# Performance work log

Measured on AMD Instinct MI355X. Metric: run time of the kernel, lower is better.

The kernel has to match this reference:

```python
import jax, jax.numpy as jnp
import numpy as np

N = 50000          # nodes
E = 400000         # random edges (self-loops added in reference, per PyG default)
IN, HID, HEADS, OUT = 20, 64, 4, 256
NEG_SLOPE = 0.2    # GATv2Conv default negative_slope
EPS = 1e-16        # PyG softmax denom epsilon


def setup_inputs() -> dict:
    key = jax.random.key(0)
    ks = jax.random.split(key, 14)
    g = lambda k, shape, scale=0.1: (jax.random.normal(k, shape, jnp.float32) * scale)
    return {
        "x": jax.random.normal(ks[0], (N, IN), jnp.float32),
        "edge_index": jax.random.randint(ks[1], (2, E), 0, N, jnp.int32),
        # layer 1: GATv2Conv(IN -> HID, heads=HEADS, concat=True)
        "W_l1": g(ks[2], (IN, HEADS * HID)),
        "b_l1": jnp.zeros((HEADS * HID,), jnp.float32),
        "W_r1": g(ks[3], (IN, HEADS * HID)),
        "b_r1": jnp.zeros((HEADS * HID,), jnp.float32),
        "att1": g(ks[4], (HEADS, HID)),
        "bias1": jnp.zeros((HEADS * HID,), jnp.float32),
        # layer 2: GATv2Conv(HEADS*HID -> OUT, heads=1, concat=False)
        "W_l2": g(ks[5], (HEADS * HID, OUT)),
        "b_l2": jnp.zeros((OUT,), jnp.float32),
        "W_r2": g(ks[6], (HEADS * HID, OUT)),
        "b_r2": jnp.zeros((OUT,), jnp.float32),
        "att2": g(ks[7], (1, OUT)),
        "bias2": jnp.zeros((OUT,), jnp.float32),
    }


def _gatv2_layer(x, src, dst, W_l, b_l, W_r, b_r, att, bias, heads, ch, concat):
    n = x.shape[0]
    x_l = (x @ W_l + b_l).reshape(n, heads, ch)  # source transform
    x_r = (x @ W_r + b_r).reshape(n, heads, ch)  # target transform
    # GATv2: e_ij = att . LeakyReLU(x_l[j] + x_r[i])   (j->i edge)
    pre = jax.nn.leaky_relu(x_l[src] + x_r[dst], NEG_SLOPE)       # [E, H, C]
    logits = jnp.einsum('ehc,hc->eh', pre, att)                    # [E, H]
    # segment softmax over destination node (self-loops guarantee nonempty)
    m = jax.ops.segment_max(logits, dst, num_segments=n)
    w = jnp.exp(logits - m[dst])
    denom = jax.ops.segment_sum(w, dst, num_segments=n)
    alpha = w / (denom[dst] + EPS)                                 # [E, H]
    out = jax.ops.segment_sum(x_l[src] * alpha[:, :, None], dst, num_segments=n)
    out = out.reshape(n, heads * ch) if concat else out.mean(axis=1)
    return out + bias


def reference(x, edge_index, W_l1, b_l1, W_r1, b_r1, att1, bias1,
              W_l2, b_l2, W_r2, b_r2, att2, bias2):
    n = x.shape[0]
    loop = jnp.arange(n, dtype=edge_index.dtype)  # PyG add_self_loops=True
    src = jnp.concatenate([edge_index[0], loop])
    dst = jnp.concatenate([edge_index[1], loop])
    h = _gatv2_layer(x, src, dst, W_l1, b_l1, W_r1, b_r1, att1, bias1, HEADS, HID, True)
    h = jax.nn.elu(h)
    out = _gatv2_layer(h, src, dst, W_l2, b_l2, W_r2, b_r2, att2, bias2, 1, OUT, False)
    return out
```

## Files before the change

kernel.cpp:

```cpp
#include <hip/hip_runtime.h>
#include <math.h>

#define CH 256
#define SCAN_BLOCK 1024
#define LOG2E 1.44269504088896f

typedef _Float16 h2 __attribute__((ext_vector_type(2)));
typedef _Float16 h4 __attribute__((ext_vector_type(4)));
typedef _Float16 f16x8 __attribute__((ext_vector_type(8)));
typedef float f32x4 __attribute__((ext_vector_type(4)));

__device__ __forceinline__ float elu(float v)   { return v > 0.f ? v : __expf(v) - 1.f; }

__device__ __forceinline__ unsigned short f2h(float f) {
    union { _Float16 h; unsigned short u; } c;
    c.h = (_Float16)f;
    return c.u;
}

__device__ __forceinline__ float edge_logit(h4 r, h2 xrlo, h2 xrhi, h2 alo, h2 ahi) {
    const h2 k = {(_Float16)0.2f, (_Float16)0.2f};
    h2 rlo = {r.x, r.y}, rhi = {r.z, r.w};
    h2 slo = rlo + xrlo;
    h2 shi = rhi + xrhi;
    slo = __builtin_elementwise_max(slo, slo * k);
    shi = __builtin_elementwise_max(shi, shi * k);
    float p = __builtin_amdgcn_fdot2(slo, alo, 0.f, false);
    return __builtin_amdgcn_fdot2(shi, ahi, p, false);
}

template<int C>
__device__ __forceinline__ float dppadd(float v) {
    int t = __builtin_amdgcn_update_dpp(0, __float_as_int(v), C, 0xf, 0xf, true);
    return v + __int_as_float(t);
}
__device__ __forceinline__ float red16(float p) {
    p = dppadd<0xB1>(p);
    p = dppadd<0x4E>(p);
    p = dppadd<0x141>(p);
    p = dppadd<0x140>(p);
    return p;
}
__device__ __forceinline__ float red64(float p) {
    p = red16(p);
    p += __shfl_xor(p, 16);
    p += __shfl_xor(p, 32);
    return p;
}

typedef const __attribute__((address_space(1))) unsigned int* gas_p;
typedef __attribute__((address_space(3))) unsigned int* las_p;
__device__ __forceinline__ void gload16(const unsigned short* g, unsigned short* l) {
    __builtin_amdgcn_global_load_lds((gas_p)g, (las_p)l, 16, 0, 0);
}

__global__ __launch_bounds__(256) void gemm1_kernel(const float* __restrict__ x,
                             const float* __restrict__ Wl, const float* __restrict__ bl,
                             const float* __restrict__ Wr, const float* __restrict__ br,
                             unsigned short* __restrict__ xl, unsigned short* __restrict__ xr, int n) {
    __shared__ float xs[64][20];
    int n0 = blockIdx.x * 64;
    int tid = threadIdx.x;
    for (int i = tid; i < 64 * 20; i += 256) {
        int m = i / 20, k = i % 20;
        int row = n0 + m;
        xs[m][k] = (row < n) ? x[(size_t)row * 20 + k] : 0.f;
    }
    int c = tid;
    float wl[20], wr[20];
#pragma unroll
    for (int k = 0; k < 20; ++k) { wl[k] = Wl[k * 256 + c]; wr[k] = Wr[k * 256 + c]; }
    float blv = bl[c], brv = br[c];
    __syncthreads();
#pragma unroll 1
    for (int g = 0; g < 8; ++g) {
        int base = g * 8;
        float al[8], ar[8];
#pragma unroll
        for (int m = 0; m < 8; ++m) { al[m] = blv; ar[m] = brv; }
#pragma unroll
        for (int k = 0; k < 20; ++k) {
            float wlv = wl[k], wrv = wr[k];
#pragma unroll
            for (int m = 0; m < 8; ++m) {
                float xv = xs[base + m][k];
                al[m] += xv * wlv;
                ar[m] += xv * wrv;
            }
        }
#pragma unroll
        for (int m = 0; m < 8; ++m) {
            int row = n0 + base + m;
            if (row < n) {
                xl[(size_t)row * 256 + c] = f2h(al[m]);
                xr[(size_t)row * 256 + c] = f2h(ar[m]);
            }
        }
    }
}

__global__ void count_deg(const int* __restrict__ ei, int* __restrict__ deg, int e) {
    int t = blockIdx.x * blockDim.x + threadIdx.x;
    if (t < e) atomicAdd(&deg[ei[e + t]], 1);
}

__global__ void scan_block_k(const int* __restrict__ deg, int* __restrict__ rowptr,
                             int* __restrict__ bsums, int n) {
    __shared__ int wsum[16];
    __shared__ int woff[17];
    int tid = threadIdx.x;
    int gi = blockIdx.x * SCAN_BLOCK + tid;
    int lane = tid & 63, wid = tid >> 6;
    int v = (gi < n) ? deg[gi] : 0;
    int incl = v;
#pragma unroll
    for (int d = 1; d < 64; d <<= 1) {
        int t = __shfl_up(incl, d, 64);
        if (lane >= d) incl += t;
    }
    if (lane == 63) wsum[wid] = incl;
    __syncthreads();
    if (tid < 16) {
        int s = wsum[tid];
#pragma unroll
        for (int d = 1; d < 16; d <<= 1) {
            int t = __shfl_up(s, d, 64);
            if (tid >= d) s += t;
        }
        woff[tid + 1] = s;
        if (tid == 0) woff[0] = 0;
    }
    __syncthreads();
    incl += woff[wid];
    if (gi < n) rowptr[gi + 1] = incl;
    if (tid == 0) bsums[blockIdx.x] = woff[16];
}

__global__ void scan_tops_k(int* bsums, int nb) {
    int tid = threadIdx.x;
    int v = (tid < nb) ? bsums[tid] : 0;
    int incl = v;
#pragma unroll
    for (int d = 1; d < 64; d <<= 1) {
        int t = __shfl_up(incl, d, 64);
        if (tid >= d) incl += t;
    }
    if (tid < nb) bsums[tid] = incl - v;
}

__global__ void scan_fix_k(int* __restrict__ rowptr, int* __restrict__ cursor,
                           const int* __restrict__ deg, const int* __restrict__ bsums, int n) {
    int gi = blockIdx.x * SCAN_BLOCK + threadIdx.x;
    if (gi >= n) return;
    int off = bsums[blockIdx.x];
    int incl = rowptr[gi + 1] + off;
    rowptr[gi + 1] = incl;
    cursor[gi] = incl - deg[gi];
    if (gi == 0) rowptr[0] = 0;
}

__global__ void scatter_k(const int* __restrict__ ei, int* __restrict__ cursor,
                          int* __restrict__ csr, int e) {
    int t = blockIdx.x * blockDim.x + threadIdx.x;
    if (t >= e) return;
    int s = ei[t], d = ei[e + t];
    int idx = atomicAdd(&cursor[d], 1);
    csr[idx] = s;
}

__global__ void fused_gat1(const unsigned short* __restrict__ xl, const unsigned short* __restrict__ xr,
                           const int* __restrict__ rowptr, const int* __restrict__ csr,
                           const float* __restrict__ att, const float* __restrict__ bias,
                           unsigned short* __restrict__ hout, int n) {
    int wid = threadIdx.x >> 6;
    int lane = threadIdx.x & 63;
    int i = blockIdx.x * 4 + wid;
    if (i >= n) return;
    h4 xr4 = ((const h4*)(xr + (size_t)i * CH))[lane];
    h2 xrlo = {xr4.x, xr4.y}, xrhi = {xr4.z, xr4.w};
    float4 a4 = ((const float4*)att)[lane];
    h2 alo = {(_Float16)(a4.x * LOG2E), (_Float16)(a4.y * LOG2E)};
    h2 ahi = {(_Float16)(a4.z * LOG2E), (_Float16)(a4.w * LOG2E)};
    h4 xli = ((const h4*)(xl + (size_t)i * CH))[lane];
    float ws = __builtin_exp2f(red16(edge_logit(xli, xrlo, xrhi, alo, ahi)));
    float l = ws;
    float4 acc = make_float4(ws * (float)xli.x, ws * (float)xli.y,
                             ws * (float)xli.z, ws * (float)xli.w);
    int beg = rowptr[i], end = rowptr[i + 1];
    int el = end - 1;
    h4 r0, r1, r2, r3;
    if (beg < end) {
        int s0 = csr[beg];
        int s1 = csr[min(beg + 1, el)];
        int s2 = csr[min(beg + 2, el)];
        int s3 = csr[min(beg + 3, el)];
        r0 = ((const h4*)(xl + (size_t)s0 * CH))[lane];
        r1 = ((const h4*)(xl + (size_t)s1 * CH))[lane];
        r2 = ((const h4*)(xl + (size_t)s2 * CH))[lane];
        r3 = ((const h4*)(xl + (size_t)s3 * CH))[lane];
    }
    int e = beg;
    for (; e + 4 <= end; e += 4) {
        h4 q0 = r0, q1 = r1, q2 = r2, q3 = r3;
        int en = e + 4;
        if (en < end) {
            int t0 = csr[en];
            int t1 = csr[min(en + 1, el)];
            int t2 = csr[min(en + 2, el)];
            int t3 = csr[min(en + 3, el)];
            r0 = ((const h4*)(xl + (size_t)t0 * CH))[lane];
            r1 = ((const h4*)(xl + (size_t)t1 * CH))[lane];
            r2 = ((const h4*)(xl + (size_t)t2 * CH))[lane];
            r3 = ((const h4*)(xl + (size_t)t3 * CH))[lane];
        }
        float w0 = __builtin_exp2f(red16(edge_logit(q0, xrlo, xrhi, alo, ahi)));
        float w1 = __builtin_exp2f(red16(edge_logit(q1, xrlo, xrhi, alo, ahi)));
        float w2 = __builtin_exp2f(red16(edge_logit(q2, xrlo, xrhi, alo, ahi)));
        float w3 = __builtin_exp2f(red16(edge_logit(q3, xrlo, xrhi, alo, ahi)));
        l += (w0 + w1) + (w2 + w3);
        acc.x += w0*(float)q0.x + w1*(float)q1.x + w2*(float)q2.x + w3*(float)q3.x;
        acc.y += w0*(float)q0.y + w1*(float)q1.y + w2*(float)q2.y + w3*(float)q3.y;
        acc.z += w0*(float)q0.z + w1*(float)q1.z + w2*(float)q2.z + w3*(float)q3.z;
        acc.w += w0*(float)q0.w + w1*(float)q1.w + w2*(float)q2.w + w3*(float)q3.w;
    }
    int cnt = end - e;
    if (cnt) {
        float p0 = red16(edge_logit(r0, xrlo, xrhi, alo, ahi));
        float p1 = red16(edge_logit(r1, xrlo, xrhi, alo, ahi));
        float p2 = red16(edge_logit(r2, xrlo, xrhi, alo, ahi));
        if (cnt < 2) p1 = -INFINITY;
        if (cnt < 3) p2 = -INFINITY;
        float w0 = __builtin_exp2f(p0), w1 = __builtin_exp2f(p1), w2 = __builtin_exp2f(p2);
        l += w0 + w1 + w2;
        acc.x += w0*(float)r0.x + w1*(float)r1.x + w2*(float)r2.x;
        acc.y += w0*(float)r0.y + w1*(float)r1.y + w2*(float)r2.y;
        acc.z += w0*(float)r0.z + w1*(float)r1.z + w2*(float)r2.z;
        acc.w += w0*(float)r0.w + w1*(float)r1.w + w2*(float)r2.w;
    }
    float inv = 1.f / l;
    float4 b4 = ((const float4*)bias)[lane];
    h4 o;
    o.x = (_Float16)elu(acc.x * inv + b4.x);
    o.y = (_Float16)elu(acc.y * inv + b4.y);
    o.z = (_Float16)elu(acc.z * inv + b4.z);
    o.w = (_Float16)elu(acc.w * inv + b4.w);
    ((h4*)(hout + (size_t)i * CH))[lane] = o;
}

__global__ void fused_gat2(const unsigned short* __restrict__ xl, const unsigned short* __restrict__ xr,
                           const int* __restrict__ rowptr, const int* __restrict__ csr,
                           const float* __restrict__ att, const float* __restrict__ bias,
                           float* __restrict__ out, int n) {
    int wid = threadIdx.x >> 6;
    int lane = threadIdx.x & 63;
    int i = blockIdx.x * 4 + wid;
    if (i >= n) return;
    h4 xr4 = ((const h4*)(xr + (size_t)i * CH))[lane];
    h2 xrlo = {xr4.x, xr4.y}, xrhi = {xr4.z, xr4.w};
    float4 a4 = ((const float4*)att)[lane];
    h2 alo = {(_Float16)(a4.x * LOG2E), (_Float16)(a4.y * LOG2E)};
    h2 ahi = {(_Float16)(a4.z * LOG2E), (_Float16)(a4.w * LOG2E)};
    h4 xli = ((const h4*)(xl + (size_t)i * CH))[lane];
    float ws = __builtin_exp2f(red64(edge_logit(xli, xrlo, xrhi, alo, ahi)));
    float l = ws;
    float4 acc = make_float4(ws * (float)xli.x, ws * (float)xli.y,
                             ws * (float)xli.z, ws * (float)xli.w);
    int beg = rowptr[i], end = rowptr[i + 1];
    int el = end - 1;
    h4 r0, r1, r2, r3;
    if (beg < end) {
        int s0 = csr[beg];
        int s1 = csr[min(beg + 1, el)];
        int s2 = csr[min(beg + 2, el)];
        int s3 = csr[min(beg + 3, el)];
        r0 = ((const h4*)(xl + (size_t)s0 * CH))[lane];
        r1 = ((const h4*)(xl + (size_t)s1 * CH))[lane];
        r2 = ((const h4*)(xl + (size_t)s2 * CH))[lane];
        r3 = ((const h4*)(xl + (size_t)s3 * CH))[lane];
    }
    int e = beg;
    for (; e + 4 <= end; e += 4) {
        h4 q0 = r0, q1 = r1, q2 = r2, q3 = r3;
        int en = e + 4;
        if (en < end) {
            int t0 = csr[en];
            int t1 = csr[min(en + 1, el)];
            int t2 = csr[min(en + 2, el)];
            int t3 = csr[min(en + 3, el)];
            r0 = ((const h4*)(xl + (size_t)t0 * CH))[lane];
            r1 = ((const h4*)(xl + (size_t)t1 * CH))[lane];
            r2 = ((const h4*)(xl + (size_t)t2 * CH))[lane];
            r3 = ((const h4*)(xl + (size_t)t3 * CH))[lane];
        }
        float w0 = __builtin_exp2f(red64(edge_logit(q0, xrlo, xrhi, alo, ahi)));
        float w1 = __builtin_exp2f(red64(edge_logit(q1, xrlo, xrhi, alo, ahi)));
        float w2 = __builtin_exp2f(red64(edge_logit(q2, xrlo, xrhi, alo, ahi)));
        float w3 = __builtin_exp2f(red64(edge_logit(q3, xrlo, xrhi, alo, ahi)));
        l += (w0 + w1) + (w2 + w3);
        acc.x += w0*(float)q0.x + w1*(float)q1.x + w2*(float)q2.x + w3*(float)q3.x;
        acc.y += w0*(float)q0.y + w1*(float)q1.y + w2*(float)q2.y + w3*(float)q3.y;
        acc.z += w0*(float)q0.z + w1*(float)q1.z + w2*(float)q2.z + w3*(float)q3.z;
        acc.w += w0*(float)q0.w + w1*(float)q1.w + w2*(float)q2.w + w3*(float)q3.w;
    }
    int cnt = end - e;
    if (cnt) {
        float p0 = red64(edge_logit(r0, xrlo, xrhi, alo, ahi));
        float p1 = red64(edge_logit(r1, xrlo, xrhi, alo, ahi));
        float p2 = red64(edge_logit(r2, xrlo, xrhi, alo, ahi));
        if (cnt < 2) p1 = -INFINITY;
        if (cnt < 3) p2 = -INFINITY;
        float w0 = __builtin_exp2f(p0), w1 = __builtin_exp2f(p1), w2 = __builtin_exp2f(p2);
        l += w0 + w1 + w2;
        acc.x += w0*(float)r0.x + w1*(float)r1.x + w2*(float)r2.x;
        acc.y += w0*(float)r0.y + w1*(float)r1.y + w2*(float)r2.y;
        acc.z += w0*(float)r0.z + w1*(float)r1.z + w2*(float)r2.z;
        acc.w += w0*(float)r0.w + w1*(float)r1.w + w2*(float)r2.w;
    }
    float inv = 1.f / l;
    float4 b4 = ((const float4*)bias)[lane];
    float4 o;
    o.x = acc.x * inv + b4.x;
    o.y = acc.y * inv + b4.y;
    o.z = acc.z * inv + b4.z;
    o.w = acc.w * inv + b4.w;
    ((float4*)(out + (size_t)i * CH))[lane] = o;
}

__global__ void wconv(const float* __restrict__ Wl2, const float* __restrict__ Wr2,
                      unsigned short* __restrict__ Wt) {
    int t = blockIdx.x * 256 + threadIdx.x;
    int z = t >> 16;
    int idx = t & 65535;
    int k = idx >> 8, nn = idx & 255;
    const float* W = z ? Wr2 : Wl2;
    Wt[z * 65536 + nn * 256 + k] = f2h(W[k * 256 + nn]);
}

#define LDE 32
__global__ __launch_bounds__(256) void gemm_mfma(
        const unsigned short* __restrict__ A,
        const unsigned short* __restrict__ Wt,
        const float* __restrict__ ba, const float* __restrict__ bb,
        unsigned short* __restrict__ Ca, unsigned short* __restrict__ Cb, int M) {
    const unsigned short* Wz = Wt + (size_t)blockIdx.z * 65536;
    const float* bias = blockIdx.z ? bb : ba;
    unsigned short* C = blockIdx.z ? Cb : Ca;

    __shared__ unsigned short As[2][128 * LDE];
    __shared__ unsigned short Bs[2][128 * LDE];

    int m0 = blockIdx.x * 128, n0 = blockIdx.y * 128;
    int tid = threadIdx.x;
    int lane = tid & 63, wid = tid >> 6;
    int wm = wid & 1, wn = wid >> 1;
    int q = lane >> 4, l15 = lane & 15;

    int lr = lane >> 2;
    int lc = (lane & 3) * 8;
    int Mm1 = M - 1;
    int ra0 = m0 + wid * 32 + lr;      if (ra0 > Mm1) ra0 = Mm1;
    int ra1 = m0 + wid * 32 + 16 + lr; if (ra1 > Mm1) ra1 = Mm1;
    const unsigned short* pa0 = A  + (size_t)ra0 * 256 + lc;
    const unsigned short* pa1 = A  + (size_t)ra1 * 256 + lc;
    const unsigned short* pb0 = Wz + (size_t)(n0 + wid * 32 + lr) * 256 + lc;
    const unsigned short* pb1 = Wz + (size_t)(n0 + wid * 32 + 16 + lr) * 256 + lc;

    f32x4 acc[4][4];
#pragma unroll
    for (int i = 0; i < 4; ++i)
#pragma unroll
        for (int j = 0; j < 4; ++j) acc[i][j] = (f32x4){0.f, 0.f, 0.f, 0.f};

#define STAGE(b, kb) do {                                   \
        int koff = (kb) * 32;                               \
        gload16(pa0 + koff, &As[b][(wid * 32) * LDE]);      \
        gload16(pa1 + koff, &As[b][(wid * 32 + 16) * LDE]); \
        gload16(pb0 + koff, &Bs[b][(wid * 32) * LDE]);      \
        gload16(pb1 + koff, &Bs[b][(wid * 32 + 16) * LDE]); \
    } while (0)

    STAGE(0, 0);
    __syncthreads();

#pragma unroll
    for (int kb = 0; kb < 8; ++kb) {
        int cur = kb & 1;
        if (kb < 7) STAGE(cur ^ 1, kb + 1);

        f16x8 af[4], bfr[4];
#pragma unroll
        for (int f = 0; f < 4; ++f)
            af[f] = *(const f16x8*)&As[cur][(wm * 64 + f * 16 + l15) * LDE + q * 8];
#pragma unroll
        for (int f = 0; f < 4; ++f)
            bfr[f] = *(const f16x8*)&Bs[cur][(wn * 64 + f * 16 + l15) * LDE + q * 8];
#pragma unroll
        for (int i = 0; i < 4; ++i)
#pragma unroll
            for (int j = 0; j < 4; ++j)
                acc[i][j] = __builtin_amdgcn_mfma_f32_16x16x32_f16(af[i], bfr[j], acc[i][j], 0, 0, 0);

        __syncthreads();
    }
#undef STAGE

#pragma unroll
    for (int j = 0; j < 4; ++j) {
        int gcol = n0 + wn * 64 + j * 16 + l15;
        float bcol = bias[gcol];
#pragma unroll
        for (int i = 0; i < 4; ++i) {
            int row = m0 + wm * 64 + i * 16 + q * 4;
#pragma unroll
            for (int rr = 0; rr < 4; ++rr) {
                int grow = row + rr;
                if (grow < M)
                    C[(size_t)grow * 256 + gcol] = f2h(acc[i][j][rr] + bcol);
            }
        }
    }
}

extern "C" void kernel_launch(void* const* d_in, const int* in_sizes, int n_in,
                              void* d_out, int out_size, void* d_ws, size_t ws_size,
                              hipStream_t stream) {
    const float* x    = (const float*)d_in[0];
    const int*   ei   = (const int*)d_in[1];
    const float* Wl1  = (const float*)d_in[2];
    const float* bl1  = (const float*)d_in[3];
    const float* Wr1  = (const float*)d_in[4];
    const float* br1  = (const float*)d_in[5];
    const float* att1 = (const float*)d_in[6];
    const float* bias1= (const float*)d_in[7];
    const float* Wl2  = (const float*)d_in[8];
    const float* bl2  = (const float*)d_in[9];
    const float* Wr2  = (const float*)d_in[10];
    const float* br2  = (const float*)d_in[11];
    const float* att2 = (const float*)d_in[12];
    const float* bias2= (const float*)d_in[13];

    int n = in_sizes[0] / 20;
    int e = in_sizes[1] / 2;
    float* out = (float*)d_out;
    size_t nch = (size_t)n * CH;

    unsigned short* buf0 = (unsigned short*)d_ws;
    unsigned short* buf1 = buf0 + nch;
    unsigned short* hbuf = buf1 + nch;
    unsigned short* wt2  = hbuf + nch;
    int* deg    = (int*)(wt2 + 2 * 65536);
    int* rowptr = deg + n;
    int* cursor = rowptr + n + 1;
    int* bsums  = cursor + n;
    int* csr    = bsums + 64;

    hipMemsetAsync(deg, 0, (size_t)n * sizeof(int), stream);

    gemm1_kernel<<<(n + 63) / 64, 256, 0, stream>>>(x, Wl1, bl1, Wr1, br1, buf0, buf1, n);

    count_deg<<<(e + 255) / 256, 256, 0, stream>>>(ei, deg, e);
    int nb = (n + SCAN_BLOCK - 1) / SCAN_BLOCK;
    scan_block_k<<<nb, SCAN_BLOCK, 0, stream>>>(deg, rowptr, bsums, n);
    scan_tops_k<<<1, 64, 0, stream>>>(bsums, nb);
    scan_fix_k<<<nb, SCAN_BLOCK, 0, stream>>>(rowptr, cursor, deg, bsums, n);
    scatter_k<<<(e + 255) / 256, 256, 0, stream>>>(ei, cursor, csr, e);

    wconv<<<512, 256, 0, stream>>>(Wl2, Wr2, wt2);

    fused_gat1<<<(n + 3) / 4, 256, 0, stream>>>(buf0, buf1, rowptr, csr, att1, bias1, hbuf, n);

    gemm_mfma<<<dim3((n + 127) / 128, 2, 2), 256, 0, stream>>>(hbuf, wt2, bl2, br2, buf0, buf1, n);

    fused_gat2<<<(n + 3) / 4, 256, 0, stream>>>(buf0, buf1, rowptr, csr, att2, bias2, out, n);
}
```

Measured before the change: 303.4 us.

## Load MFMA operands directly from global into registers, dropping LDS staging

Replaces the LDS double-buffered staging in the layer-2 MFMA GEMM with direct per-lane global loads of f16x8 fragments into registers, software-pipelined one k-step ahead. This removes the shared-memory round trip and the per-iteration __syncthreads barriers. In exchange, each wave fetches its own A and B fragments, so data shared across waves (A rows reused by the two wn waves, B rows by the two wm waves) is reloaded from global/L2 rather than shared through LDS. Register pressure also rises from holding next-step fragments.

```diff
diff --git a/kernel.cpp b/kernel.cpp
--- a/kernel.cpp
+++ b/kernel.cpp
@@ -46,12 +46,6 @@
     p += __shfl_xor(p, 16);
     p += __shfl_xor(p, 32);
     return p;
-}
-
-typedef const __attribute__((address_space(1))) unsigned int* gas_p;
-typedef __attribute__((address_space(3))) unsigned int* las_p;
-__device__ __forceinline__ void gload16(const unsigned short* g, unsigned short* l) {
-    __builtin_amdgcn_global_load_lds((gas_p)g, (las_p)l, 16, 0, 0);
 }
 
 __global__ __launch_bounds__(256) void gemm1_kernel(const float* __restrict__ x,
@@ -336,7 +330,6 @@
     Wt[z * 65536 + nn * 256 + k] = f2h(W[k * 256 + nn]);
 }
 
-#define LDE 32
 __global__ __launch_bounds__(256) void gemm_mfma(
         const unsigned short* __restrict__ A,
         const unsigned short* __restrict__ Wt,
@@ -346,24 +339,23 @@
     const float* bias = blockIdx.z ? bb : ba;
     unsigned short* C = blockIdx.z ? Cb : Ca;
 
-    __shared__ unsigned short As[2][128 * LDE];
-    __shared__ unsigned short Bs[2][128 * LDE];
-
     int m0 = blockIdx.x * 128, n0 = blockIdx.y * 128;
     int tid = threadIdx.x;
     int lane = tid & 63, wid = tid >> 6;
     int wm = wid & 1, wn = wid >> 1;
     int q = lane >> 4, l15 = lane & 15;
 
-    int lr = lane >> 2;
-    int lc = (lane & 3) * 8;
+    const unsigned short* pa[4];
+    const unsigned short* pb[4];
     int Mm1 = M - 1;
-    int ra0 = m0 + wid * 32 + lr;      if (ra0 > Mm1) ra0 = Mm1;
-    int ra1 = m0 + wid * 32 + 16 + lr; if (ra1 > Mm1) ra1 = Mm1;
-    const unsigned short* pa0 = A  + (size_t)ra0 * 256 + lc;
-    const unsigned short* pa1 = A  + (size_t)ra1 * 256 + lc;
-    const unsigned short* pb0 = Wz + (size_t)(n0 + wid * 32 + lr) * 256 + lc;
-    const unsigned short* pb1 = Wz + (size_t)(n0 + wid * 32 + 16 + lr) * 256 + lc;
+#pragma unroll
+    for (int i = 0; i < 4; ++i) {
+        int arow = m0 + wm * 64 + i * 16 + l15;
+        if (arow > Mm1) arow = Mm1;
+        pa[i] = A + (size_t)arow * 256 + q * 8;
+        int brow = n0 + wn * 64 + i * 16 + l15;
+        pb[i] = Wz + (size_t)brow * 256 + q * 8;
+    }
 
     f32x4 acc[4][4];
 #pragma unroll
@@ -371,38 +363,31 @@
 #pragma unroll
         for (int j = 0; j < 4; ++j) acc[i][j] = (f32x4){0.f, 0.f, 0.f, 0.f};
 
-#define STAGE(b, kb) do {                                   \
-        int koff = (kb) * 32;                               \
-        gload16(pa0 + koff, &As[b][(wid * 32) * LDE]);      \
-        gload16(pa1 + koff, &As[b][(wid * 32 + 16) * LDE]); \
-        gload16(pb0 + koff, &Bs[b][(wid * 32) * LDE]);      \
-        gload16(pb1 + koff, &Bs[b][(wid * 32 + 16) * LDE]); \
-    } while (0)
-
-    STAGE(0, 0);
-    __syncthreads();
+    f16x8 a_cur[4], b_cur[4], a_nxt[4], b_nxt[4];
+#pragma unroll
+    for (int i = 0; i < 4; ++i) {
+        a_cur[i] = *(const f16x8*)(pa[i]);
+        b_cur[i] = *(const f16x8*)(pb[i]);
+    }
 
 #pragma unroll
     for (int kb = 0; kb < 8; ++kb) {
-        int cur = kb & 1;
-        if (kb < 7) STAGE(cur ^ 1, kb + 1);
-
-        f16x8 af[4], bfr[4];
-#pragma unroll
-        for (int f = 0; f < 4; ++f)
-            af[f] = *(const f16x8*)&As[cur][(wm * 64 + f * 16 + l15) * LDE + q * 8];
-#pragma unroll
-        for (int f = 0; f < 4; ++f)
-            bfr[f] = *(const f16x8*)&Bs[cur][(wn * 64 + f * 16 + l15) * LDE + q * 8];
+        if (kb < 7) {
+            int off = (kb + 1) * 32;
+#pragma unroll
+            for (int i = 0; i < 4; ++i) {
+                a_nxt[i] = *(const f16x8*)(pa[i] + off);
+                b_nxt[i] = *(const f16x8*)(pb[i] + off);
+            }
+        }
 #pragma unroll
         for (int i = 0; i < 4; ++i)
 #pragma unroll
             for (int j = 0; j < 4; ++j)
-                acc[i][j] = __builtin_amdgcn_mfma_f32_16x16x32_f16(af[i], bfr[j], acc[i][j], 0, 0, 0);
-
-        __syncthreads();
-    }
-#undef STAGE
+                acc[i][j] = __builtin_amdgcn_mfma_f32_16x16x32_f16(a_cur[i], b_cur[j], acc[i][j], 0, 0, 0);
+#pragma unroll
+        for (int i = 0; i < 4; ++i) { a_cur[i] = a_nxt[i]; b_cur[i] = b_nxt[i]; }
+    }
 
 #pragma unroll
     for (int j = 0; j < 4; ++j) {
```

Result: slower. 336.9 us (+11.1%).
